# Kernel tuning notes

Hardware: AMD Instinct MI355X
Metric: run time of the kernel (lower is better)

Reference implementation:

```python
import jax, jax.numpy as jnp
import numpy as np

T = 16                       # sample_duration
FG_THRESH, BG_HI, BG_LO = 0.5, 0.5, 0.1
ROIS_PER_IMAGE, FG_PER_IMAGE = 128, 32   # conf.TRAIN.BATCH_SIZE, round(0.25*128)
STDS = jnp.tile(jnp.array([0.1, 0.1, 0.2, 0.2], jnp.float32), T)  # BBOX_NORMALIZE_STDS tiled; means are 0


def _tube_iou(rois, gts):
    # rois [b,M,T,4], gts [b,K,T,4] -> mean per-frame IoU over non-empty frames [b,M,K]
    r = rois[:, :, None]             # [b,M,1,T,4]
    g = gts[:, None]                 # [b,1,K,T,4]
    iw = jnp.clip(jnp.minimum(r[..., 2], g[..., 2]) - jnp.maximum(r[..., 0], g[..., 0]) + 1.0, 0.0)
    ih = jnp.clip(jnp.minimum(r[..., 3], g[..., 3]) - jnp.maximum(r[..., 1], g[..., 1]) + 1.0, 0.0)
    inter = iw * ih
    ar = (r[..., 2] - r[..., 0] + 1.0) * (r[..., 3] - r[..., 1] + 1.0)
    ag = (g[..., 2] - g[..., 0] + 1.0) * (g[..., 3] - g[..., 1] + 1.0)
    r_empty = jnp.all(r == 0.0, -1)
    g_empty = jnp.all(g == 0.0, -1)
    iou = jnp.where(r_empty | g_empty, 0.0, inter / (ar + ag - inter))
    valid = ~(r_empty & g_empty)
    return iou.sum(-1) / jnp.maximum(valid.sum(-1), 1).astype(iou.dtype)


def _bbox_transform(ex, gt):
    ew = ex[..., 2] - ex[..., 0] + 1.0
    eh = ex[..., 3] - ex[..., 1] + 1.0
    ecx = ex[..., 0] + 0.5 * ew
    ecy = ex[..., 1] + 0.5 * eh
    gw = gt[..., 2] - gt[..., 0] + 1.0
    gh = gt[..., 3] - gt[..., 1] + 1.0
    gcx = gt[..., 0] + 0.5 * gw
    gcy = gt[..., 1] + 0.5 * gh
    return jnp.stack([(gcx - ecx) / ew, (gcy - ecy) / eh,
                      jnp.log(gw / ew), jnp.log(gh / eh)], axis=-1)


def _sample_one(ov, lab, key):
    # ov, lab: [M]; jit-safe fg/bg sampling matching the torch control flow
    M = ov.shape[0]
    k1, k2, k3, k4 = jax.random.split(key, 4)
    fg = ov >= FG_THRESH
    bg = (ov < BG_HI) & (ov >= BG_LO)
    fg_num = fg.sum()
    bg_num = bg.sum()
    # random permutation with fg (resp. bg) indices first
    order_fg = jnp.argsort(jnp.where(fg, jax.random.uniform(k1, (M,)), 2.0))
    order_bg = jnp.argsort(jnp.where(bg, jax.random.uniform(k2, (M,)), 2.0))
    fg_this = jnp.where(bg_num > 0, jnp.minimum(FG_PER_IMAGE, fg_num),
                        jnp.where(fg_num > 0, ROIS_PER_IMAGE, 0))
    r = jnp.arange(ROIS_PER_IMAGE)
    fg_repl = order_fg[(jax.random.uniform(k3, (ROIS_PER_IMAGE,)) * jnp.maximum(fg_num, 1)).astype(jnp.int32)]
    fg_idx = jnp.where(bg_num > 0, order_fg[r], fg_repl)  # no-replacement when bg exists, else with replacement
    bg_idx = order_bg[(jax.random.uniform(k4, (ROIS_PER_IMAGE,)) * jnp.maximum(bg_num, 1)).astype(jnp.int32)]
    is_fg = r < fg_this
    keep = jnp.where(is_fg, fg_idx, bg_idx)
    return keep, jnp.where(is_fg, lab[keep], 0.0)


def _forward(all_tubes, gt_boxes, gt_tubes_all):
    b, N, _ = all_tubes.shape
    A = gt_boxes.shape[1]
    # gt tube coords + label of first nonzero-labelled frame
    gt_tubes = gt_boxes[..., :4].reshape(b, A, T * 4)
    fr_lab = gt_boxes[..., 4]                                    # [b,A,T]
    has = jnp.any(fr_lab != 0, axis=2)
    first = jnp.argmax(fr_lab != 0, axis=2)
    labels_gt = jnp.where(has, jnp.take_along_axis(fr_lab, first[..., None], 2)[..., 0], 0.0)
    # scatter tube coords into frames [round(start), round(end)] (vectorized mask-scatter)
    sf = jnp.round(all_tubes[..., 3]).astype(jnp.int32)[..., None]
    ef = jnp.round(all_tubes[..., 6]).astype(jnp.int32)[..., None]
    f = jnp.arange(T)[None, None]
    fmask = ((f >= sf) & (f <= ef)).astype(all_tubes.dtype)      # [b,N,T]
    coords = all_tubes[..., jnp.array([1, 2, 4, 5])]             # [b,N,4]
    all_rois = fmask[..., None] * coords[:, :, None, :]          # [b,N,T,4]
    off = jnp.broadcast_to(jnp.arange(b, dtype=all_rois.dtype)[:, None, None], (b, N, 1))
    all_rois = jnp.concatenate([off, all_rois.reshape(b, N, T * 4)], axis=2)
    # append gt boxes/tubes as extra proposals (batch col = 0)
    gt_app = jnp.concatenate([jnp.zeros((b, A, 1), all_rois.dtype), gt_tubes], axis=2)
    all_rois = jnp.concatenate([all_rois, gt_app], axis=1)       # [b,N+A,1+4T]
    gt_tubes_app = jnp.concatenate([jnp.zeros((b, A, 1), all_tubes.dtype), gt_tubes_all[..., :-1]], axis=2)
    all_tubes_c = jnp.concatenate([all_tubes, gt_tubes_app], axis=1)  # [b,N+A,7]
    # IoU overlaps + gt assignment
    ov = _tube_iou(all_rois[..., 1:].reshape(b, N + A, T, 4),
                   gt_tubes.reshape(b, A, T, 4))                 # [b,N+A,A]
    max_ov = ov.max(axis=2)
    gt_asg = ov.argmax(axis=2)
    labels = jnp.take_along_axis(labels_gt, gt_asg, axis=1)      # [b,N+A]
    # fg/bg sampling (fixed key -> deterministic)
    keys = jax.random.split(jax.random.key(42), b)
    keep, labels_b = jax.vmap(_sample_one)(max_ov, labels, keys)  # [b,R]
    rois_b = jnp.take_along_axis(all_rois, keep[..., None], axis=1)
    rois_b = rois_b.at[..., 0].set(jnp.arange(b, dtype=rois_b.dtype)[:, None])
    tubes_b = jnp.take_along_axis(all_tubes_c, keep[..., None], axis=1)
    tubes_b = tubes_b.at[..., 0].set(jnp.arange(b, dtype=tubes_b.dtype)[:, None])
    asg_k = jnp.take_along_axis(gt_asg, keep, axis=1)
    gt_rois_b = jnp.take_along_axis(gt_tubes, asg_k[..., None], axis=1)  # [b,R,4T]
    tgt = _bbox_transform(rois_b[..., 1:].reshape(b, ROIS_PER_IMAGE, T, 4),
                          gt_rois_b.reshape(b, ROIS_PER_IMAGE, T, 4)).reshape(b, ROIS_PER_IMAGE, T * 4)
    tgt = tgt / STDS
    pos = (labels_b > 0)[..., None]
    bbox_targets = jnp.where(pos, tgt, 0.0)
    inside = jnp.where(pos, jnp.ones_like(tgt), 0.0)
    outside = (inside > 0).astype(tgt.dtype)
    return rois_b, tubes_b, labels_b, bbox_targets, inside, outside


def setup_inputs() -> dict:
    key = jax.random.key(0)
    ks = jax.random.split(key, 9)
    b, N, A = 8, 20000, 5
    x1 = jax.random.uniform(ks[0], (b, N), minval=0.0, maxval=200.0)
    y1 = jax.random.uniform(ks[1], (b, N), minval=0.0, maxval=200.0)
    x2 = x1 + jax.random.uniform(ks[2], (b, N), minval=8.0, maxval=120.0)
    y2 = y1 + jax.random.uniform(ks[3], (b, N), minval=8.0, maxval=120.0)
    sf = jax.random.randint(ks[4], (b, N), 0, T).astype(jnp.float32)
    ef = jnp.minimum(sf + jax.random.randint(ks[5], (b, N), 0, T).astype(jnp.float32), T - 1.0)
    bidx = jnp.broadcast_to(jnp.arange(b, dtype=jnp.float32)[:, None], (b, N))
    all_tubes = jnp.stack([bidx, x1, y1, sf, x2, y2, ef], axis=-1)
    gx1 = jax.random.uniform(ks[6], (b, A, T), minval=0.0, maxval=200.0)
    gy1 = jax.random.uniform(ks[7], (b, A, T), minval=0.0, maxval=200.0)
    gx2 = gx1 + 60.0
    gy2 = gy1 + 60.0
    glab = jax.random.randint(ks[8], (b, A), 1, 21).astype(jnp.float32)[..., None]
    gt_boxes = jnp.stack([gx1, gy1, gx2, gy2, jnp.broadcast_to(glab, (b, A, T))], axis=-1)
    gt_tubes_all = jnp.concatenate([
        jnp.zeros((b, A, 1)), gx1.min(-1, keepdims=True), gy1.min(-1, keepdims=True),
        jnp.zeros((b, A, 1)), gx2.max(-1, keepdims=True), gy2.max(-1, keepdims=True),
        jnp.full((b, A, 1), T - 1.0)], axis=-1).astype(jnp.float32)
    return {"all_tubes": all_tubes, "gt_boxes": gt_boxes, "gt_tubes_all": gt_tubes_all}


def reference(all_tubes, gt_boxes, gt_tubes_all):
    return _forward(all_tubes, gt_boxes, gt_tubes_all)
```

## Files before the change

### kernel.cpp

```cpp
#include <hip/hip_runtime.h>
#include <stdint.h>

#define T 16
#define NB 8
#define NROI 20000
#define NA 5
#define MM (NROI + NA)
#define MMPAD 20224
#define RPI 128
#define FGPI 32
#define NBLK 79
#define NBLK2 20
#define SORTCAP 32768
#define CSTRIDE 32

__host__ __device__ __forceinline__ void tf2x32(uint32_t k0, uint32_t k1,
                                                uint32_t x0, uint32_t x1,
                                                uint32_t& o0, uint32_t& o1) {
  uint32_t ks2 = k0 ^ k1 ^ 0x1BD11BDAu;
  x0 += k0; x1 += k1;
#define ROUND(r) { x0 += x1; x1 = (x1 << (r)) | (x1 >> (32 - (r))); x1 ^= x0; }
  ROUND(13) ROUND(15) ROUND(26) ROUND(6)
  x0 += k1; x1 += ks2 + 1u;
  ROUND(17) ROUND(29) ROUND(16) ROUND(24)
  x0 += ks2; x1 += k0 + 2u;
  ROUND(13) ROUND(15) ROUND(26) ROUND(6)
  x0 += k0; x1 += k1 + 3u;
  ROUND(17) ROUND(29) ROUND(16) ROUND(24)
  x0 += k1; x1 += ks2 + 4u;
  ROUND(13) ROUND(15) ROUND(26) ROUND(6)
  x0 += ks2; x1 += k0 + 5u;
#undef ROUND
  o0 = x0; o1 = x1;
}

__device__ __forceinline__ uint32_t rbits32(uint32_t k0, uint32_t k1, uint32_t i) {
  uint32_t a, b; tf2x32(k0, k1, 0u, i, a, b); return a ^ b;
}
__device__ __forceinline__ float uni01(uint32_t bits) {
  return __uint_as_float((bits >> 9) | 0x3f800000u) - 1.0f;
}

struct Keys { uint32_t k[NB][4][2]; };

__global__ __launch_bounds__(256) void k_iou(const float* __restrict__ tubes,
                                             const float* __restrict__ gtb,
                                             float* __restrict__ ov) {
  int img = blockIdx.y;
  int a = blockIdx.z;
  int b = blockIdx.x;
  int tid = threadIdx.x;
  int n = b * 256 + tid;
  bool valid = n < MM;
  int nn = valid ? n : MM - 1;
  bool isroi = nn < NROI;

  __shared__ float tub[256 * 7];
  __shared__ float4 g4[NA][T];
  __shared__ float gar[NA][T];
  {
    int rcnt = min(256, NROI - b * 256);
    int f4cnt = (rcnt * 7) >> 2;
    const float4* src = (const float4*)(tubes + (size_t)img * NROI * 7 + (size_t)b * 256 * 7);
    float4* dst = (float4*)tub;
    for (int i = tid; i < f4cnt; i += 256) dst[i] = src[i];
  }
  for (int i = tid; i < NA * T; i += 256) {
    int aa = i / T, t = i - aa * T;
    const float* p = gtb + (((size_t)img * NA + aa) * T + t) * 5;
    float4 v = make_float4(p[0], p[1], p[2], p[3]);
    g4[aa][t] = v;
    gar[aa][t] = (v.z - v.x + 1.0f) * (v.w - v.y + 1.0f);
  }
  __syncthreads();

  float s = 0.0f;
  if (isroi) {
    const float* p = &tub[tid * 7];
    float rx1 = p[1], ry1 = p[2], rx2 = p[4], ry2 = p[5];
    int sf = (int)rintf(p[3]), ef = (int)rintf(p[6]);
    float rar = (rx2 - rx1 + 1.0f) * (ry2 - ry1 + 1.0f);
#pragma unroll
    for (int t = 0; t < T; ++t) {
      float4 gg = g4[a][t]; float ag = gar[a][t];
      float iw = fmaxf(fminf(rx2, gg.z) - fmaxf(rx1, gg.x) + 1.0f, 0.0f);
      float ih = fmaxf(fminf(ry2, gg.w) - fmaxf(ry1, gg.y) + 1.0f, 0.0f);
      float inter = iw * ih;
      float q = inter / (rar + ag - inter);
      s += ((t >= sf) && (t <= ef)) ? q : 0.0f;
    }
  } else {
    int ga = nn - NROI;
#pragma unroll
    for (int t = 0; t < T; ++t) {
      float4 e = g4[ga][t]; float ar = gar[ga][t];
      float4 gg = g4[a][t]; float ag = gar[a][t];
      float iw = fmaxf(fminf(e.z, gg.z) - fmaxf(e.x, gg.x) + 1.0f, 0.0f);
      float ih = fmaxf(fminf(e.w, gg.w) - fmaxf(e.y, gg.y) + 1.0f, 0.0f);
      float inter = iw * ih;
      s += inter / (ar + ag - inter);
    }
  }
  if (valid) ov[((size_t)img * NA + a) * MMPAD + n] = s / 16.0f;
}

__global__ __launch_bounds__(1024) void k_classify(const float* __restrict__ ov,
                                                   unsigned char* __restrict__ asg,
                                                   uint64_t* __restrict__ slots,
                                                   int* __restrict__ cnts2,
                                                   int* __restrict__ mins2,
                                                   Keys keys) {
  int img = blockIdx.y;
  int b = blockIdx.x;
  int tid = threadIdx.x;
  int n = b * 1024 + tid;
  bool valid = n < MM;
  int nn = valid ? n : MM - 1;
  int lane = tid & 63;
  int w = tid >> 6;

  const float* base_ov = ov + (size_t)img * NA * MMPAD + nn;
  float o0 = base_ov[0 * MMPAD];
  float o1 = base_ov[1 * MMPAD];
  float o2 = base_ov[2 * MMPAD];
  float o3 = base_ov[3 * MMPAD];
  float o4 = base_ov[4 * MMPAD];
  float best = o0; int barg = 0;
  if (o1 > best) { best = o1; barg = 1; }
  if (o2 > best) { best = o2; barg = 2; }
  if (o3 > best) { best = o3; barg = 3; }
  if (o4 > best) { best = o4; barg = 4; }

  if (valid) asg[(size_t)img * MM + n] = (unsigned char)barg;

  bool isfg = valid && (best >= 0.5f);
  bool isbg = valid && (best < 0.5f) && (best >= 0.1f);

  __shared__ int wcnt[16][2];
  __shared__ int wmn[16][2];
  unsigned long long mfg = __ballot(isfg);
  unsigned long long mbg = __ballot(isbg);
  unsigned long long mnf = __ballot(valid && !isfg);
  unsigned long long mnb = __ballot(valid && !isbg);
  int wavebase = b * 1024 + w * 64;
  if (lane == 0) {
    wcnt[w][0] = __popcll(mfg);
    wcnt[w][1] = __popcll(mbg);
    wmn[w][0] = mnf ? (wavebase + __ffsll(mnf) - 1) : 0x7FFFFFFF;
    wmn[w][1] = mnb ? (wavebase + __ffsll(mnb) - 1) : 0x7FFFFFFF;
  }
  __syncthreads();

  if (tid == 0) {
    int tf = 0, tb = 0, mf = 0x7FFFFFFF, mb = 0x7FFFFFFF;
#pragma unroll
    for (int w2 = 0; w2 < 16; ++w2) {
      tf += wcnt[w2][0]; tb += wcnt[w2][1];
      mf = min(mf, wmn[w2][0]); mb = min(mb, wmn[w2][1]);
    }
    int idx = img * NBLK2 + b;
    cnts2[idx]                = tf;
    cnts2[NB * NBLK2 + idx]   = tb;
    mins2[idx]                = mf;
    mins2[NB * NBLK2 + idx]   = mb;
  }

  int pf = 0, pb = 0;
  for (int w2 = 0; w2 < w; ++w2) { pf += wcnt[w2][0]; pb += wcnt[w2][1]; }
  unsigned long long below = (1ULL << lane) - 1ULL;
  uint64_t* slotF = slots + (size_t)(img * 2 + 0) * SORTCAP + b * 1024;
  uint64_t* slotB = slots + (size_t)(img * 2 + 1) * SORTCAP + b * 1024;
  if (isfg) {
    int pos = pf + __popcll(mfg & below);
    uint32_t m = rbits32(keys.k[img][0][0], keys.k[img][0][1], (uint32_t)n) >> 9;
    slotF[pos] = ((uint64_t)m << 32) | (uint32_t)n;
  }
  if (isbg) {
    int pos = pb + __popcll(mbg & below);
    uint32_t m = rbits32(keys.k[img][1][0], keys.k[img][1][1], (uint32_t)n) >> 9;
    slotB[pos] = ((uint64_t)m << 32) | (uint32_t)n;
  }
}

__global__ __launch_bounds__(1024) void k_sort(uint64_t* __restrict__ slots,
                                               const int* __restrict__ cnts2,
                                               const int* __restrict__ mins2,
                                               int* __restrict__ counts) {
  __shared__ uint64_t buf[8192];
  __shared__ int scnt[NBLK2], spref[NBLK2 + 1], smn[NBLK2];
  __shared__ int stot;
  int list = blockIdx.x;
  int img = list >> 1;
  int which = list & 1;
  int tid = threadIdx.x;
  uint64_t* arr = slots + (size_t)(img * 2 + which) * SORTCAP;
  const int* cn = cnts2 + which * NB * NBLK2 + img * NBLK2;
  const int* mn = mins2 + which * NB * NBLK2 + img * NBLK2;

  if (tid < NBLK2) { scnt[tid] = cn[tid]; smn[tid] = mn[tid]; }
  __syncthreads();
  if (tid == 0) {
    int acc = 0, mmn = 0x7FFFFFFF;
#pragma unroll
    for (int bb = 0; bb < NBLK2; ++bb) {
      spref[bb] = acc; acc += scnt[bb]; mmn = min(mmn, smn[bb]);
    }
    spref[NBLK2] = acc; stot = acc;
    counts[img * CSTRIDE + which] = acc;
    counts[img * CSTRIDE + 2 + which] = mmn;
  }
  __syncthreads();
  int cnt = stot;
  if (cnt == 0) return;
  int n = 2; while (n < cnt) n <<= 1;

  if (n <= 8192) {
    for (int s = tid; s < NBLK2 * 1024; s += 1024) {
      int bb = s >> 10, i = s & 1023;
      if (i < scnt[bb]) buf[spref[bb] + i] = arr[s];
    }
    for (int i = cnt + tid; i < n; i += 1024) buf[i] = ~0ULL;
    __syncthreads();
    for (int k = 2; k <= n; k <<= 1) {
      for (int j = k >> 1; j; j >>= 1) {
        for (int i = tid; i < n; i += 1024) {
          int ixj = i ^ j;
          if (ixj > i) {
            uint64_t a = buf[i], bv = buf[ixj];
            bool up = (i & k) == 0;
            if (up ? (a > bv) : (a < bv)) { buf[i] = bv; buf[ixj] = a; }
          }
        }
        __syncthreads();
      }
    }
    for (int i = tid; i < cnt; i += 1024) arr[i] = buf[i];
  } else {
    for (int bb = 0; bb < NBLK2; ++bb) {
      uint64_t v = 0; int c = scnt[bb];
      if (tid < c) v = arr[bb * 1024 + tid];
      __syncthreads();
      if (tid < c) arr[spref[bb] + tid] = v;
      __syncthreads();
    }
    for (int i = cnt + tid; i < n; i += 1024) arr[i] = ~0ULL;
    __syncthreads();
    for (int k = 2; k <= n; k <<= 1) {
      for (int j = k >> 1; j; j >>= 1) {
        for (int i = tid; i < n; i += 1024) {
          int ixj = i ^ j;
          if (ixj > i) {
            uint64_t a = arr[i], bv = arr[ixj];
            bool up = (i & k) == 0;
            if (up ? (a > bv) : (a < bv)) { arr[i] = bv; arr[ixj] = a; }
          }
        }
        __syncthreads();
      }
    }
  }
}

__global__ __launch_bounds__(256) void k_sample(const float* __restrict__ tubes,
                                                const float* __restrict__ gtb,
                                                const float* __restrict__ gta,
                                                const unsigned char* __restrict__ asg,
                                                const uint64_t* __restrict__ slots,
                                                const int* __restrict__ counts,
                                                Keys keys,
                                                float* __restrict__ out) {
  int img = blockIdx.x;
  int tid = threadIdx.x;
  __shared__ int s_keep[RPI];
  __shared__ int s_ak[RPI];
  __shared__ float s_lab[RPI];

  float* o_rois = out;
  float* o_tub = out + (size_t)NB * RPI * 65;
  float* o_lab = o_tub + (size_t)NB * RPI * 7;
  float* o_tgt = o_lab + (size_t)NB * RPI;
  float* o_in  = o_tgt + (size_t)NB * RPI * 64;
  float* o_ou  = o_in  + (size_t)NB * RPI * 64;

  if (tid < RPI) {
    int r = tid;
    int cb = img * CSTRIDE;
    int fg_num = counts[cb + 0], bg_num = counts[cb + 1];
    int min_nonfg = counts[cb + 2];
    int min_nonbg = counts[cb + 3];

    float u3 = uni01(rbits32(keys.k[img][2][0], keys.k[img][2][1], (uint32_t)r));
    float u4 = uni01(rbits32(keys.k[img][3][0], keys.k[img][3][1], (uint32_t)r));

    int fg_this = (bg_num > 0) ? min(FGPI, fg_num) : (fg_num > 0 ? RPI : 0);
    const uint64_t* fga = slots + (size_t)(img * 2 + 0) * SORTCAP;
    const uint64_t* bga = slots + (size_t)(img * 2 + 1) * SORTCAP;

    int fg_idx;
    if (bg_num > 0) {
      fg_idx = (int)(uint32_t)(fga[r] & 0xffffffffULL);
    } else {
      int q = (int)(u3 * (float)max(fg_num, 1));
      fg_idx = (q >= fg_num)
                 ? ((fg_num >= MM) ? (int)(uint32_t)(fga[MM - 1] & 0xffffffffULL) : min_nonfg)
                 : (int)(uint32_t)(fga[q] & 0xffffffffULL);
    }
    int qb = (int)(u4 * (float)max(bg_num, 1));
    int bg_idx = (qb >= bg_num)
                   ? ((bg_num >= MM) ? (int)(uint32_t)(bga[MM - 1] & 0xffffffffULL) : min_nonbg)
                   : (int)(uint32_t)(bga[qb] & 0xffffffffULL);

    bool is_fg = r < fg_this;
    int keep = is_fg ? fg_idx : bg_idx;
    int ak = asg[(size_t)img * MM + keep];
    float glab = gtb[(((size_t)img * NA + ak) * T + 0) * 5 + 4];
    float lab = is_fg ? glab : 0.0f;

    s_keep[r] = keep; s_ak[r] = ak; s_lab[r] = lab;

    size_t row = (size_t)img * RPI + r;
    float* pt = o_tub + row * 7;
    o_rois[row * 65] = (float)img;
    pt[0] = (float)img;
    if (keep < NROI) {
      const float* p = tubes + ((size_t)img * NROI + keep) * 7;
#pragma unroll
      for (int c = 1; c < 7; ++c) pt[c] = p[c];
    } else {
      const float* p = gta + ((size_t)img * NA + (keep - NROI)) * 7;
#pragma unroll
      for (int c = 1; c < 7; ++c) pt[c] = p[c - 1];
    }
    o_lab[row] = lab;
  }
  __syncthreads();

  for (int i = tid; i < RPI * T; i += 256) {
    int rl = i >> 4;
    int t = i & 15;
    size_t row = (size_t)img * RPI + rl;
    int keep = s_keep[rl];
    int ak = s_ak[rl];
    float lab = s_lab[rl];
    bool pos = lab > 0.0f;
    float posf = pos ? 1.0f : 0.0f;

    float ex1, ey1, ex2, ey2;
    if (keep < NROI) {
      const float* p = tubes + ((size_t)img * NROI + keep) * 7;
      int sf = (int)rintf(p[3]), ef = (int)rintf(p[6]);
      bool in = (t >= sf) && (t <= ef);
      ex1 = in ? p[1] : 0.0f; ey1 = in ? p[2] : 0.0f;
      ex2 = in ? p[4] : 0.0f; ey2 = in ? p[5] : 0.0f;
    } else {
      const float* p = gtb + (((size_t)img * NA + (keep - NROI)) * T + t) * 5;
      ex1 = p[0]; ey1 = p[1]; ex2 = p[2]; ey2 = p[3];
    }

    float* pr = o_rois + row * 65 + 1 + 4 * t;
    pr[0] = ex1; pr[1] = ey1; pr[2] = ex2; pr[3] = ey2;

    const float* gp = gtb + (((size_t)img * NA + ak) * T + t) * 5;
    float gx1 = gp[0], gy1 = gp[1], gx2 = gp[2], gy2 = gp[3];
    float ew = ex2 - ex1 + 1.0f, eh = ey2 - ey1 + 1.0f;
    float ecx = ex1 + 0.5f * ew, ecy = ey1 + 0.5f * eh;
    float gw = gx2 - gx1 + 1.0f, gh = gy2 - gy1 + 1.0f;
    float gcx = gx1 + 0.5f * gw, gcy = gy1 + 0.5f * gh;
    float t0 = ((gcx - ecx) / ew) / 0.1f;
    float t1 = ((gcy - ecy) / eh) / 0.1f;
    float t2 = logf(gw / ew) / 0.2f;
    float t3 = logf(gh / eh) / 0.2f;

    *(float4*)(o_tgt + row * 64 + 4 * t) =
        make_float4(pos ? t0 : 0.0f, pos ? t1 : 0.0f, pos ? t2 : 0.0f, pos ? t3 : 0.0f);
    float4 pf4 = make_float4(posf, posf, posf, posf);
    *(float4*)(o_in + row * 64 + 4 * t) = pf4;
    *(float4*)(o_ou + row * 64 + 4 * t) = pf4;
  }
}

extern "C" void kernel_launch(void* const* d_in, const int* in_sizes, int n_in,
                              void* d_out, int out_size, void* d_ws, size_t ws_size,
                              hipStream_t stream) {
  const float* tubes = (const float*)d_in[0];
  const float* gtb   = (const float*)d_in[1];
  const float* gta   = (const float*)d_in[2];
  float* out = (float*)d_out;
  char* ws = (char*)d_ws;

  Keys keys;
  for (int img = 0; img < NB; ++img) {
    uint32_t r0, r1; tf2x32(0u, 42u, 0u, (uint32_t)img, r0, r1);
    for (int j = 0; j < 4; ++j) {
      uint32_t a, b; tf2x32(r0, r1, 0u, (uint32_t)j, a, b);
      keys.k[img][j][0] = a; keys.k[img][j][1] = b;
    }
  }

  int* counts = (int*)ws;
  int* cnts2  = (int*)(ws + 1024);
  int* mins2  = (int*)(ws + 2304);
  unsigned char* asg = (unsigned char*)(ws + 3584);
  uint64_t* slots = (uint64_t*)(ws + 163624);
  float* ov = (float*)(ws + 4357928);

  dim3 gI(NBLK, NB, NA);
  k_iou<<<gI, 256, 0, stream>>>(tubes, gtb, ov);
  dim3 gC(NBLK2, NB);
  k_classify<<<gC, 1024, 0, stream>>>(ov, asg, slots, cnts2, mins2, keys);
  k_sort<<<16, 1024, 0, stream>>>(slots, cnts2, mins2, counts);
  k_sample<<<NB, 256, 0, stream>>>(tubes, gtb, gta, asg, slots, counts, keys, out);
}
```

Baseline: 48.65 us.

## Fuse sort and sample kernels, pack IoU argmax via atomicMax

The IoU kernel now writes a packed (overlap bits, anchor index) 64-bit key with atomicMax, so the per-ROI max and argmax are reduced in place. The classify kernel then reads one word instead of five overlaps, and the separate assignment array is gone. The sort and sample kernels are merged: each of the 16 blocks sorts its fg or bg list in LDS (now up to 16K entries) and directly emits the output rows it owns. This saves a launch, a global round-trip of the sorted list, and the counts buffer. In exchange it adds a memset, atomic contention, and a much larger LDS footprint per block.

```diff
diff --git a/kernel.cpp b/kernel.cpp
--- a/kernel.cpp
+++ b/kernel.cpp
@@ -12,7 +12,7 @@
 #define NBLK 79
 #define NBLK2 20
 #define SORTCAP 32768
-#define CSTRIDE 32
+#define LCAP 16384
 
 __host__ __device__ __forceinline__ void tf2x32(uint32_t k0, uint32_t k1,
                                                 uint32_t x0, uint32_t x1,
@@ -45,7 +45,7 @@
 
 __global__ __launch_bounds__(256) void k_iou(const float* __restrict__ tubes,
                                              const float* __restrict__ gtb,
-                                             float* __restrict__ ov) {
+                                             unsigned long long* __restrict__ pk) {
   int img = blockIdx.y;
   int a = blockIdx.z;
   int b = blockIdx.x;
@@ -101,11 +101,15 @@
       s += inter / (ar + ag - inter);
     }
   }
-  if (valid) ov[((size_t)img * NA + a) * MMPAD + n] = s / 16.0f;
-}
-
-__global__ __launch_bounds__(1024) void k_classify(const float* __restrict__ ov,
-                                                   unsigned char* __restrict__ asg,
+  if (valid) {
+    float ovv = s / 16.0f;
+    unsigned long long pkv = ((unsigned long long)__float_as_uint(ovv) << 3)
+                           | (unsigned long long)(7 - a);
+    atomicMax(&pk[(size_t)img * MMPAD + n], pkv);
+  }
+}
+
+__global__ __launch_bounds__(1024) void k_classify(const unsigned long long* __restrict__ pk,
                                                    uint64_t* __restrict__ slots,
                                                    int* __restrict__ cnts2,
                                                    int* __restrict__ mins2,
@@ -119,19 +123,8 @@
   int lane = tid & 63;
   int w = tid >> 6;
 
-  const float* base_ov = ov + (size_t)img * NA * MMPAD + nn;
-  float o0 = base_ov[0 * MMPAD];
-  float o1 = base_ov[1 * MMPAD];
-  float o2 = base_ov[2 * MMPAD];
-  float o3 = base_ov[3 * MMPAD];
-  float o4 = base_ov[4 * MMPAD];
-  float best = o0; int barg = 0;
-  if (o1 > best) { best = o1; barg = 1; }
-  if (o2 > best) { best = o2; barg = 2; }
-  if (o3 > best) { best = o3; barg = 3; }
-  if (o4 > best) { best = o4; barg = 4; }
-
-  if (valid) asg[(size_t)img * MM + n] = (unsigned char)barg;
+  unsigned long long p = pk[(size_t)img * MMPAD + nn];
+  float best = __uint_as_float((uint32_t)(p >> 3));
 
   bool isfg = valid && (best >= 0.5f);
   bool isbg = valid && (best < 0.5f) && (best >= 0.1f);
@@ -182,60 +175,74 @@
   }
 }
 
-__global__ __launch_bounds__(1024) void k_sort(uint64_t* __restrict__ slots,
-                                               const int* __restrict__ cnts2,
-                                               const int* __restrict__ mins2,
-                                               int* __restrict__ counts) {
-  __shared__ uint64_t buf[8192];
-  __shared__ int scnt[NBLK2], spref[NBLK2 + 1], smn[NBLK2];
-  __shared__ int stot;
+__global__ __launch_bounds__(1024) void k_sortsample(const float* __restrict__ tubes,
+                                                     const float* __restrict__ gtb,
+                                                     const float* __restrict__ gta,
+                                                     const unsigned long long* __restrict__ pk,
+                                                     uint64_t* __restrict__ slots,
+                                                     const int* __restrict__ cnts2,
+                                                     const int* __restrict__ mins2,
+                                                     Keys keys,
+                                                     float* __restrict__ out) {
+  __shared__ uint64_t buf[LCAP];
+  __shared__ int scnt[NBLK2], spref[NBLK2 + 1];
+  __shared__ int s_tot, s_oth, s_mn;
+  __shared__ int s_keep[RPI];
+  __shared__ int s_ak[RPI];
+  __shared__ float s_lab[RPI];
+  __shared__ unsigned char s_own[RPI];
+
   int list = blockIdx.x;
   int img = list >> 1;
   int which = list & 1;
   int tid = threadIdx.x;
   uint64_t* arr = slots + (size_t)(img * 2 + which) * SORTCAP;
   const int* cn = cnts2 + which * NB * NBLK2 + img * NBLK2;
+  const int* co = cnts2 + (1 - which) * NB * NBLK2 + img * NBLK2;
   const int* mn = mins2 + which * NB * NBLK2 + img * NBLK2;
 
-  if (tid < NBLK2) { scnt[tid] = cn[tid]; smn[tid] = mn[tid]; }
+  if (tid < NBLK2) scnt[tid] = cn[tid];
   __syncthreads();
   if (tid == 0) {
-    int acc = 0, mmn = 0x7FFFFFFF;
+    int acc = 0, mmn = 0x7FFFFFFF, oth = 0;
 #pragma unroll
     for (int bb = 0; bb < NBLK2; ++bb) {
-      spref[bb] = acc; acc += scnt[bb]; mmn = min(mmn, smn[bb]);
-    }
-    spref[NBLK2] = acc; stot = acc;
-    counts[img * CSTRIDE + which] = acc;
-    counts[img * CSTRIDE + 2 + which] = mmn;
-  }
-  __syncthreads();
-  int cnt = stot;
-  if (cnt == 0) return;
-  int n = 2; while (n < cnt) n <<= 1;
-
-  if (n <= 8192) {
+      spref[bb] = acc; acc += scnt[bb];
+      mmn = min(mmn, mn[bb]); oth += co[bb];
+    }
+    spref[NBLK2] = acc; s_tot = acc; s_mn = mmn; s_oth = oth;
+  }
+  __syncthreads();
+  int cnt = s_tot, min_non = s_mn;
+  int fg_num = (which == 0) ? cnt : s_oth;
+  int bg_num = (which == 0) ? s_oth : cnt;
+
+  int n2 = 2; while (n2 < cnt) n2 <<= 1;
+  bool ldsPath = (n2 <= LCAP);
+
+  if (cnt > 0 && ldsPath) {
     for (int s = tid; s < NBLK2 * 1024; s += 1024) {
       int bb = s >> 10, i = s & 1023;
       if (i < scnt[bb]) buf[spref[bb] + i] = arr[s];
     }
-    for (int i = cnt + tid; i < n; i += 1024) buf[i] = ~0ULL;
+    for (int i = cnt + tid; i < n2; i += 1024) buf[i] = ~0ULL;
     __syncthreads();
-    for (int k = 2; k <= n; k <<= 1) {
-      for (int j = k >> 1; j; j >>= 1) {
-        for (int i = tid; i < n; i += 1024) {
-          int ixj = i ^ j;
-          if (ixj > i) {
-            uint64_t a = buf[i], bv = buf[ixj];
-            bool up = (i & k) == 0;
-            if (up ? (a > bv) : (a < bv)) { buf[i] = bv; buf[ixj] = a; }
+    if (cnt > 1) {
+      for (int k = 2; k <= n2; k <<= 1) {
+        for (int j = k >> 1; j; j >>= 1) {
+          for (int i = tid; i < n2; i += 1024) {
+            int ixj = i ^ j;
+            if (ixj > i) {
+              uint64_t a = buf[i], bv = buf[ixj];
+              bool up = (i & k) == 0;
+              if (up ? (a > bv) : (a < bv)) { buf[i] = bv; buf[ixj] = a; }
+            }
           }
+          __syncthreads();
         }
-        __syncthreads();
       }
     }
-    for (int i = tid; i < cnt; i += 1024) arr[i] = buf[i];
-  } else {
+  } else if (cnt > 1) {
     for (int bb = 0; bb < NBLK2; ++bb) {
       uint64_t v = 0; int c = scnt[bb];
       if (tid < c) v = arr[bb * 1024 + tid];
@@ -243,11 +250,11 @@
       if (tid < c) arr[spref[bb] + tid] = v;
       __syncthreads();
     }
-    for (int i = cnt + tid; i < n; i += 1024) arr[i] = ~0ULL;
+    for (int i = cnt + tid; i < n2; i += 1024) arr[i] = ~0ULL;
     __syncthreads();
-    for (int k = 2; k <= n; k <<= 1) {
+    for (int k = 2; k <= n2; k <<= 1) {
       for (int j = k >> 1; j; j >>= 1) {
-        for (int i = tid; i < n; i += 1024) {
+        for (int i = tid; i < n2; i += 1024) {
           int ixj = i ^ j;
           if (ixj > i) {
             uint64_t a = arr[i], bv = arr[ixj];
@@ -259,21 +266,7 @@
       }
     }
   }
-}
-
-__global__ __launch_bounds__(256) void k_sample(const float* __restrict__ tubes,
-                                                const float* __restrict__ gtb,
-                                                const float* __restrict__ gta,
-                                                const unsigned char* __restrict__ asg,
-                                                const uint64_t* __restrict__ slots,
-                                                const int* __restrict__ counts,
-                                                Keys keys,
-                                                float* __restrict__ out) {
-  int img = blockIdx.x;
-  int tid = threadIdx.x;
-  __shared__ int s_keep[RPI];
-  __shared__ int s_ak[RPI];
-  __shared__ float s_lab[RPI];
+  __syncthreads();
 
   float* o_rois = out;
   float* o_tub = out + (size_t)NB * RPI * 65;
@@ -282,61 +275,63 @@
   float* o_in  = o_tgt + (size_t)NB * RPI * 64;
   float* o_ou  = o_in  + (size_t)NB * RPI * 64;
 
+  int fg_this = (bg_num > 0) ? min(FGPI, fg_num) : (fg_num > 0 ? RPI : 0);
+
+#define MY_AT(i) (ldsPath ? (int)(uint32_t)(buf[i] & 0xffffffffULL) : (int)(uint32_t)(arr[i] & 0xffffffffULL))
+
   if (tid < RPI) {
     int r = tid;
-    int cb = img * CSTRIDE;
-    int fg_num = counts[cb + 0], bg_num = counts[cb + 1];
-    int min_nonfg = counts[cb + 2];
-    int min_nonbg = counts[cb + 3];
-
-    float u3 = uni01(rbits32(keys.k[img][2][0], keys.k[img][2][1], (uint32_t)r));
-    float u4 = uni01(rbits32(keys.k[img][3][0], keys.k[img][3][1], (uint32_t)r));
-
-    int fg_this = (bg_num > 0) ? min(FGPI, fg_num) : (fg_num > 0 ? RPI : 0);
-    const uint64_t* fga = slots + (size_t)(img * 2 + 0) * SORTCAP;
-    const uint64_t* bga = slots + (size_t)(img * 2 + 1) * SORTCAP;
-
-    int fg_idx;
-    if (bg_num > 0) {
-      fg_idx = (int)(uint32_t)(fga[r] & 0xffffffffULL);
-    } else {
-      int q = (int)(u3 * (float)max(fg_num, 1));
-      fg_idx = (q >= fg_num)
-                 ? ((fg_num >= MM) ? (int)(uint32_t)(fga[MM - 1] & 0xffffffffULL) : min_nonfg)
-                 : (int)(uint32_t)(fga[q] & 0xffffffffULL);
-    }
-    int qb = (int)(u4 * (float)max(bg_num, 1));
-    int bg_idx = (qb >= bg_num)
-                   ? ((bg_num >= MM) ? (int)(uint32_t)(bga[MM - 1] & 0xffffffffULL) : min_nonbg)
-                   : (int)(uint32_t)(bga[qb] & 0xffffffffULL);
-
     bool is_fg = r < fg_this;
-    int keep = is_fg ? fg_idx : bg_idx;
-    int ak = asg[(size_t)img * MM + keep];
-    float glab = gtb[(((size_t)img * NA + ak) * T + 0) * 5 + 4];
-    float lab = is_fg ? glab : 0.0f;
-
-    s_keep[r] = keep; s_ak[r] = ak; s_lab[r] = lab;
-
-    size_t row = (size_t)img * RPI + r;
-    float* pt = o_tub + row * 7;
-    o_rois[row * 65] = (float)img;
-    pt[0] = (float)img;
-    if (keep < NROI) {
-      const float* p = tubes + ((size_t)img * NROI + keep) * 7;
-#pragma unroll
-      for (int c = 1; c < 7; ++c) pt[c] = p[c];
-    } else {
-      const float* p = gta + ((size_t)img * NA + (keep - NROI)) * 7;
-#pragma unroll
-      for (int c = 1; c < 7; ++c) pt[c] = p[c - 1];
-    }
-    o_lab[row] = lab;
-  }
-  __syncthreads();
-
-  for (int i = tid; i < RPI * T; i += 256) {
+    bool own = (is_fg == (which == 0));
+    s_own[r] = own ? 1 : 0;
+    if (own) {
+      int keep;
+      if (which == 0) {
+        if (bg_num > 0) {
+          keep = MY_AT(r);
+        } else {
+          float u3 = uni01(rbits32(keys.k[img][2][0], keys.k[img][2][1], (uint32_t)r));
+          int q = (int)(u3 * (float)max(fg_num, 1));
+          keep = (q >= fg_num)
+                   ? ((fg_num >= MM) ? MY_AT(MM - 1) : min_non)
+                   : MY_AT(q);
+        }
+      } else {
+        float u4 = uni01(rbits32(keys.k[img][3][0], keys.k[img][3][1], (uint32_t)r));
+        int qb = (int)(u4 * (float)max(bg_num, 1));
+        keep = (qb >= bg_num)
+                 ? ((bg_num >= MM) ? MY_AT(MM - 1) : min_non)
+                 : MY_AT(qb);
+      }
+
+      unsigned long long pkv = pk[(size_t)img * MMPAD + keep];
+      int ak = 7 - (int)(pkv & 7ULL);
+      float glab = gtb[(((size_t)img * NA + ak) * T + 0) * 5 + 4];
+      float lab = is_fg ? glab : 0.0f;
+      s_keep[r] = keep; s_ak[r] = ak; s_lab[r] = lab;
+
+      size_t row = (size_t)img * RPI + r;
+      float* pt = o_tub + row * 7;
+      o_rois[row * 65] = (float)img;
+      pt[0] = (float)img;
+      if (keep < NROI) {
+        const float* p = tubes + ((size_t)img * NROI + keep) * 7;
+#pragma unroll
+        for (int cc = 1; cc < 7; ++cc) pt[cc] = p[cc];
+      } else {
+        const float* p = gta + ((size_t)img * NA + (keep - NROI)) * 7;
+#pragma unroll
+        for (int cc = 1; cc < 7; ++cc) pt[cc] = p[cc - 1];
+      }
+      o_lab[row] = lab;
+    }
+  }
+#undef MY_AT
+  __syncthreads();
+
+  for (int i = tid; i < RPI * T; i += 1024) {
     int rl = i >> 4;
+    if (!s_own[rl]) continue;
     int t = i & 15;
     size_t row = (size_t)img * RPI + rl;
     int keep = s_keep[rl];
@@ -397,17 +392,15 @@
     }
   }
 
-  int* counts = (int*)ws;
-  int* cnts2  = (int*)(ws + 1024);
-  int* mins2  = (int*)(ws + 2304);
-  unsigned char* asg = (unsigned char*)(ws + 3584);
-  uint64_t* slots = (uint64_t*)(ws + 163624);
-  float* ov = (float*)(ws + 4357928);
-
+  int* cnts2 = (int*)ws;
+  int* mins2 = (int*)(ws + 1280);
+  unsigned long long* pk = (unsigned long long*)(ws + 4096);
+  uint64_t* slots = (uint64_t*)(ws + 1298432);
+
+  hipMemsetAsync(pk, 0, (size_t)NB * MMPAD * 8, stream);
   dim3 gI(NBLK, NB, NA);
-  k_iou<<<gI, 256, 0, stream>>>(tubes, gtb, ov);
+  k_iou<<<gI, 256, 0, stream>>>(tubes, gtb, pk);
   dim3 gC(NBLK2, NB);
-  k_classify<<<gC, 1024, 0, stream>>>(ov, asg, slots, cnts2, mins2, keys);
-  k_sort<<<16, 1024, 0, stream>>>(slots, cnts2, mins2, counts);
-  k_sample<<<NB, 256, 0, stream>>>(tubes, gtb, gta, asg, slots, counts, keys, out);
-}
+  k_classify<<<gC, 1024, 0, stream>>>(pk, slots, cnts2, mins2, keys);
+  k_sortsample<<<16, 1024, 0, stream>>>(tubes, gtb, gta, pk, slots, cnts2, mins2, keys, out);
+}
```

Result: no change. 48.35 us (-0.6%).
